# Kernel tuning notes

Measured on AMD Instinct MI355X. Metric: run time of the kernel, lower is better.

Reference implementation:

```python
import jax, jax.numpy as jnp
import numpy as np

N_NODES = 100000
N_EDGES = 1600000
D = 128


def _sage_conv(x, src, dst, W_l, b_l, W_r, num_nodes):
    # gather source-node features along edges, mean-aggregate at destination
    msg_sum = jax.ops.segment_sum(x[src], dst, num_segments=num_nodes)  # [N, D]
    cnt = jax.ops.segment_sum(jnp.ones((src.shape[0], 1), x.dtype), dst,
                              num_segments=num_nodes)                   # [N, 1]
    agg = msg_sum / jnp.maximum(cnt, 1.0)
    # PyG SAGEConv: lin_l(aggregated) + bias + lin_r(self), root linear has no bias
    return agg @ W_l + b_l + x @ W_r


def setup_inputs() -> dict:
    key = jax.random.key(0)
    ks = jax.random.split(key, 8)
    scale = 1.0 / np.sqrt(D)
    x = jax.random.normal(ks[0], (N_NODES, D), dtype=jnp.float32)
    edge_index = jax.random.randint(ks[1], (2, N_EDGES), 0, N_NODES, dtype=jnp.int64)
    W_l1 = jax.random.normal(ks[2], (D, D), dtype=jnp.float32) * scale
    b_l1 = jnp.zeros((D,), dtype=jnp.float32)
    W_r1 = jax.random.normal(ks[3], (D, D), dtype=jnp.float32) * scale
    W_l2 = jax.random.normal(ks[4], (D, D), dtype=jnp.float32) * scale
    b_l2 = jnp.zeros((D,), dtype=jnp.float32)
    W_r2 = jax.random.normal(ks[5], (D, D), dtype=jnp.float32) * scale
    return {"x": x, "edge_index": edge_index, "W_l1": W_l1, "b_l1": b_l1,
            "W_r1": W_r1, "W_l2": W_l2, "b_l2": b_l2, "W_r2": W_r2}


def reference(x, edge_index, W_l1, b_l1, W_r1, W_l2, b_l2, W_r2):
    src, dst = edge_index[0], edge_index[1]
    n = x.shape[0]
    h = jax.nn.relu(_sage_conv(x, src, dst, W_l1, b_l1, W_r1, n))
    out = _sage_conv(h, src, dst, W_l2, b_l2, W_r2, n)
    return out
```

## Files before the change

### kernel.cpp

```cpp
#include <hip/hip_runtime.h>
#include <hip/hip_bf16.h>

#define DF 128
#define BSH 7
#define BNODES (1 << BSH)
#define SRCBITS 17
#define SRCMASK ((1u << SRCBITS) - 1u)
#define NBLK 512
#define SLABSH 13
#define NKEYS (BNODES * 16)
#define EBCAP 2560
#define CURSTR 16

typedef __attribute__((ext_vector_type(8))) short short8;
typedef __attribute__((ext_vector_type(4))) float floatx4;

__device__ __forceinline__ unsigned short f2bf(float f) {
  unsigned u = __float_as_uint(f);
  u += 0x7fffu + ((u >> 16) & 1u);
  return (unsigned short)(u >> 16);
}
__device__ __forceinline__ float bflo(unsigned u) { return __uint_as_float(u << 16); }
__device__ __forceinline__ float bfhi(unsigned u) { return __uint_as_float(u & 0xffff0000u); }


__global__ __launch_bounds__(256) void fused_prep(const int* __restrict__ src,
                                                  const int* __restrict__ dst,
                                                  int* __restrict__ cur,
                                                  unsigned* __restrict__ ebuf,
                                                  int e, int nb, int chunk,
                                                  const float* __restrict__ x,
                                                  unsigned short* __restrict__ xb, int n4,
                                                  const float* __restrict__ W0,
                                                  const float* __restrict__ W1,
                                                  const float* __restrict__ W2,
                                                  const float* __restrict__ W3,
                                                  unsigned short* __restrict__ wf) {
  int bid = blockIdx.x, t = threadIdx.x;
  if (bid < NBLK) {
    __shared__ int cnt[1024];
    __shared__ int runb[1024];
    for (int b = t; b < nb; b += 256) cnt[b] = 0;
    __syncthreads();
    int s = bid * chunk, en = min(e, s + chunk);
    int sv[13], dv[13];
    int cntl = 0;
#pragma unroll
    for (int j = 0; j < 13; ++j) {
      int i = s + t + j * 256;
      if (i < en) { sv[j] = src[i]; dv[j] = dst[i]; cntl = j + 1; }
    }
#pragma unroll
    for (int j = 0; j < 13; ++j)
      if (j < cntl) atomicAdd(&cnt[dv[j] >> BSH], 1);
    __syncthreads();
    for (int b = t; b < nb; b += 256) {
      int c = cnt[b];
      runb[b] = (c > 0) ? (b * EBCAP + atomicAdd(&cur[b * CURSTR], c)) : 0;
    }
    __syncthreads();
#pragma unroll
    for (int j = 0; j < 13; ++j)
      if (j < cntl) {
        int d = dv[j];
        int p = atomicAdd(&runb[d >> BSH], 1);
        ebuf[p] = ((unsigned)(d & (BNODES - 1)) << SRCBITS) | (unsigned)sv[j];
      }
  } else if (bid < NBLK + 256) {
    int bb = bid - NBLK;
    int m = bb >> 6;
    const float* W = (m == 0) ? W0 : (m == 1) ? W1 : (m == 2) ? W2 : W3;
    int tt = (bb & 63) * 256 + t;
    int j = tt & 7, lane = (tt >> 3) & 63, ktnt = tt >> 9;
    int nt = ktnt & 7, kt = ktnt >> 3;
    int k = kt * 32 + (lane >> 4) * 8 + j;
    int ncol = nt * 16 + (lane & 15);
    wf[m * 16384 + tt] = f2bf(W[k * DF + ncol]);
  } else {
    int i = (bid - NBLK - 256) * 256 + t;
    if (i < n4) {
      float4 v = ((const float4*)x)[i];
      union { unsigned short u[4]; uint2 d; } o;
      o.u[0] = f2bf(v.x); o.u[1] = f2bf(v.y); o.u[2] = f2bf(v.z); o.u[3] = f2bf(v.w);
      ((uint2*)xb)[i] = o.d;
    }
  }
}

__global__ __launch_bounds__(256) void fill_fine(const unsigned* __restrict__ ebuf,
                                                 const int* __restrict__ cend,
                                                 int* __restrict__ rs,
                                                 int* __restrict__ csr, int n) {
  __shared__ int hist[NKEYS];
  __shared__ int cur[NKEYS];
  __shared__ int wsum[4];
  int b = blockIdx.x;
  int t = threadIdx.x;
  for (int i = t; i < NKEYS; i += 256) hist[i] = 0;
  __syncthreads();
  int s = b * EBCAP, e = s + cend[b * CURSTR];
  for (int i = s + t; i < e; i += 256) {
    unsigned p = ebuf[i];
    int key = (int)((p >> SRCBITS) << 4) | (int)((p & SRCMASK) >> SLABSH);
    atomicAdd(&hist[key], 1);
  }
  __syncthreads();
  int v[8], sum = 0;
#pragma unroll
  for (int j = 0; j < 8; ++j) { v[j] = hist[t * 8 + j]; sum += v[j]; }
  int lane = t & 63, wid = t >> 6;
  int S = sum;
#pragma unroll
  for (int o = 1; o < 64; o <<= 1) {
    int u = __shfl_up(S, o);
    if (lane >= o) S += u;
  }
  if (lane == 63) wsum[wid] = S;
  __syncthreads();
  if (wid == 0 && lane < 4) {
    int ws = wsum[lane];
#pragma unroll
    for (int o = 1; o < 4; o <<= 1) {
      int u = __shfl_up(ws, o);
      if (lane >= o) ws += u;
    }
    wsum[lane] = ws;
  }
  __syncthreads();
  int base = (S - sum) + ((wid > 0) ? wsum[wid - 1] : 0);
#pragma unroll
  for (int j = 0; j < 8; ++j) { cur[t * 8 + j] = base; base += v[j]; }
  __syncthreads();
  if (t < BNODES) {
    int g = (b << BSH) + t;
    if (g < n) {
      int endoff = (t == BNODES - 1) ? (e - s) : cur[(t + 1) << 4];
      rs[g] = s + endoff;
    }
  }
  __syncthreads();
  for (int i = s + t; i < e; i += 256) {
    unsigned p = ebuf[i];
    int key = (int)((p >> SRCBITS) << 4) | (int)((p & SRCMASK) >> SLABSH);
    int r = atomicAdd(&cur[key], 1);
    csr[s + r] = (int)(p & SRCMASK);
  }
}

__global__ __launch_bounds__(256) void agg_pull(const uint4* __restrict__ feat,
                                                const int* __restrict__ rs,
                                                const int* __restrict__ csr,
                                                uint4* __restrict__ out, int n) {
  int node = (blockIdx.x * 256 + threadIdx.x) >> 6;
  if (node >= n) return;
  int lane = threadIdx.x & 63;
  int g = lane >> 4, l = lane & 15;
  int s = (node & (BNODES - 1)) ? rs[node - 1] : (node >> BSH) * EBCAP;
  int e = rs[node];
  float a0 = 0.f, a1 = 0.f, a2 = 0.f, a3 = 0.f;
  float a4 = 0.f, a5 = 0.f, a6 = 0.f, a7 = 0.f;
  int em1 = e - 1;
  for (int i = s; i < e; i += 16) {
    int i0 = i + g, i1 = i + g + 4, i2 = i + g + 8, i3 = i + g + 12;
    int c0 = csr[min(i0, em1)];
    int c1 = csr[min(i1, em1)];
    int c2 = csr[min(i2, em1)];
    int c3 = csr[min(i3, em1)];
    uint4 u0 = feat[c0 * 16 + l];
    uint4 u1 = feat[c1 * 16 + l];
    uint4 u2 = feat[c2 * 16 + l];
    uint4 u3 = feat[c3 * 16 + l];
    if (i0 >= e) { u0.x = 0u; u0.y = 0u; u0.z = 0u; u0.w = 0u; }
    if (i1 >= e) { u1.x = 0u; u1.y = 0u; u1.z = 0u; u1.w = 0u; }
    if (i2 >= e) { u2.x = 0u; u2.y = 0u; u2.z = 0u; u2.w = 0u; }
    if (i3 >= e) { u3.x = 0u; u3.y = 0u; u3.z = 0u; u3.w = 0u; }
    a0 += bflo(u0.x); a1 += bfhi(u0.x); a2 += bflo(u0.y); a3 += bfhi(u0.y);
    a4 += bflo(u0.z); a5 += bfhi(u0.z); a6 += bflo(u0.w); a7 += bfhi(u0.w);
    a0 += bflo(u1.x); a1 += bfhi(u1.x); a2 += bflo(u1.y); a3 += bfhi(u1.y);
    a4 += bflo(u1.z); a5 += bfhi(u1.z); a6 += bflo(u1.w); a7 += bfhi(u1.w);
    a0 += bflo(u2.x); a1 += bfhi(u2.x); a2 += bflo(u2.y); a3 += bfhi(u2.y);
    a4 += bflo(u2.z); a5 += bfhi(u2.z); a6 += bflo(u2.w); a7 += bfhi(u2.w);
    a0 += bflo(u3.x); a1 += bfhi(u3.x); a2 += bflo(u3.y); a3 += bfhi(u3.y);
    a4 += bflo(u3.z); a5 += bfhi(u3.z); a6 += bflo(u3.w); a7 += bfhi(u3.w);
  }
  a0 += __shfl_xor(a0, 16); a0 += __shfl_xor(a0, 32);
  a1 += __shfl_xor(a1, 16); a1 += __shfl_xor(a1, 32);
  a2 += __shfl_xor(a2, 16); a2 += __shfl_xor(a2, 32);
  a3 += __shfl_xor(a3, 16); a3 += __shfl_xor(a3, 32);
  a4 += __shfl_xor(a4, 16); a4 += __shfl_xor(a4, 32);
  a5 += __shfl_xor(a5, 16); a5 += __shfl_xor(a5, 32);
  a6 += __shfl_xor(a6, 16); a6 += __shfl_xor(a6, 32);
  a7 += __shfl_xor(a7, 16); a7 += __shfl_xor(a7, 32);
  if (g == 0) {
    float sc = 1.0f / (float)max(e - s, 1);
    uint4 o;
    o.x = (unsigned)f2bf(a0 * sc) | ((unsigned)f2bf(a1 * sc) << 16);
    o.y = (unsigned)f2bf(a2 * sc) | ((unsigned)f2bf(a3 * sc) << 16);
    o.z = (unsigned)f2bf(a4 * sc) | ((unsigned)f2bf(a5 * sc) << 16);
    o.w = (unsigned)f2bf(a6 * sc) | ((unsigned)f2bf(a7 * sc) << 16);
    out[node * 16 + l] = o;
  }
}

__global__ __launch_bounds__(256) void gemm_sage(const unsigned short* __restrict__ Aagg,
                                                 const unsigned short* __restrict__ Aself,
                                                 const unsigned short* __restrict__ WFl,
                                                 const unsigned short* __restrict__ WFr,
                                                 const float* __restrict__ bias,
                                                 void* __restrict__ outp, int n,
                                                 int relu_out_bf16) {
  __shared__ unsigned short Wsl[DF * DF];
  __shared__ unsigned short Wsr[DF * DF];
  int t = threadIdx.x;
  {
    const uint4* wl4 = (const uint4*)WFl;
    const uint4* wr4 = (const uint4*)WFr;
    uint4* sl4 = (uint4*)Wsl;
    uint4* sr4 = (uint4*)Wsr;
#pragma unroll
    for (int i = 0; i < 8; ++i) {
      sl4[i * 256 + t] = wl4[i * 256 + t];
      sr4[i * 256 + t] = wr4[i * 256 + t];
    }
  }
  __syncthreads();

  int wave = t >> 6;
  int lane = t & 63;
  int l16 = lane & 15, quad = lane >> 4;
  int rbase = (blockIdx.x * 4 + wave) * 32;
  if (rbase >= n) return;

  floatx4 acc[2][8];
#pragma unroll
  for (int a = 0; a < 2; ++a)
#pragma unroll
    for (int b = 0; b < 8; ++b) acc[a][b] = (floatx4)0.0f;

  int r0 = min(rbase + l16, n - 1);
  int r1 = min(rbase + 16 + l16, n - 1);

#pragma unroll
  for (int s = 0; s < 2; ++s) {
    const unsigned short* A = s ? Aself : Aagg;
    const unsigned short* W = s ? Wsr : Wsl;
    short8 a0[4], a1[4];
#pragma unroll
    for (int kt = 0; kt < 4; ++kt) {
      a0[kt] = *(const short8*)(A + r0 * DF + kt * 32 + quad * 8);
      a1[kt] = *(const short8*)(A + r1 * DF + kt * 32 + quad * 8);
    }
#pragma unroll
    for (int kt = 0; kt < 4; ++kt) {
#pragma unroll
      for (int nt = 0; nt < 8; ++nt) {
        short8 bf = *(const short8*)(W + (((kt * 8 + nt) * 64) + lane) * 8);
        acc[0][nt] = __builtin_amdgcn_mfma_f32_16x16x32_bf16(a0[kt], bf, acc[0][nt], 0, 0, 0);
        acc[1][nt] = __builtin_amdgcn_mfma_f32_16x16x32_bf16(a1[kt], bf, acc[1][nt], 0, 0, 0);
      }
    }
  }

  float bv[8];
#pragma unroll
  for (int nt = 0; nt < 8; ++nt) bv[nt] = bias[nt * 16 + l16];

  if (relu_out_bf16) {
    unsigned short* O = (unsigned short*)outp;
#pragma unroll
    for (int rb = 0; rb < 2; ++rb)
#pragma unroll
      for (int i = 0; i < 4; ++i) {
        int row = rbase + rb * 16 + quad * 4 + i;
        if (row < n) {
#pragma unroll
          for (int nt = 0; nt < 8; ++nt) {
            float v = acc[rb][nt][i] + bv[nt];
            O[row * DF + nt * 16 + l16] = f2bf(fmaxf(v, 0.0f));
          }
        }
      }
  } else {
    float* O = (float*)outp;
#pragma unroll
    for (int rb = 0; rb < 2; ++rb)
#pragma unroll
      for (int i = 0; i < 4; ++i) {
        int row = rbase + rb * 16 + quad * 4 + i;
        if (row < n) {
#pragma unroll
          for (int nt = 0; nt < 8; ++nt)
            O[row * DF + nt * 16 + l16] = acc[rb][nt][i] + bv[nt];
        }
      }
  }
}


extern "C" void kernel_launch(void* const* d_in, const int* in_sizes, int n_in,
                              void* d_out, int out_size, void* d_ws, size_t ws_size,
                              hipStream_t stream) {
  const float* x   = (const float*)d_in[0];
  const int*   ei  = (const int*)d_in[1];
  const float* Wl1 = (const float*)d_in[2];
  const float* bl1 = (const float*)d_in[3];
  const float* Wr1 = (const float*)d_in[4];
  const float* Wl2 = (const float*)d_in[5];
  const float* bl2 = (const float*)d_in[6];
  const float* Wr2 = (const float*)d_in[7];

  int n = in_sizes[0] / DF;
  int e = in_sizes[1] / 2;
  const int* srcv = ei;
  const int* dstv = ei + e;
  int nb = (n + BNODES - 1) >> BSH;
  int chunk = (e + NBLK - 1) / NBLK;

  char* ws = (char*)d_ws;
  size_t off = 0;
  auto alloc = [&](size_t bytes) {
    void* p = ws + off;
    off = (off + bytes + 255) & ~(size_t)255;
    return p;
  };
  int* cur   = (int*)alloc((size_t)nb * CURSTR * 4);
  int* rs    = (int*)alloc((size_t)n * 4);
  unsigned* ebuf = (unsigned*)alloc((size_t)nb * EBCAP * 4);
  int* csr   = (int*)alloc((size_t)nb * EBCAP * 4);
  unsigned short* xb   = (unsigned short*)alloc((size_t)n * DF * 2);
  unsigned short* hb   = (unsigned short*)alloc((size_t)n * DF * 2);
  unsigned short* aggb = (unsigned short*)alloc((size_t)n * DF * 2);
  unsigned short* wf   = (unsigned short*)alloc(4 * DF * DF * 2);
  unsigned short* wfl1 = wf;
  unsigned short* wfr1 = wf + 16384;
  unsigned short* wfl2 = wf + 32768;
  unsigned short* wfr2 = wf + 49152;

  int n4 = n * DF / 4;
  int cb = (n4 + 255) / 256;
  hipMemsetAsync(cur, 0, (size_t)nb * CURSTR * 4, stream);
  fused_prep<<<NBLK + 256 + cb, 256, 0, stream>>>(srcv, dstv, cur, ebuf, e, nb, chunk,
                                                  x, xb, n4, Wl1, Wr1, Wl2, Wr2, wf);
  fill_fine<<<nb, 256, 0, stream>>>(ebuf, cur, rs, csr, n);

  agg_pull<<<(n * 64 + 255) / 256, 256, 0, stream>>>((const uint4*)xb, rs, csr,
                                                     (uint4*)aggb, n);
  gemm_sage<<<(n + 127) / 128, 256, 0, stream>>>(aggb, xb, wfl1, wfr1, bl1, hb, n, 1);
  agg_pull<<<(n * 64 + 255) / 256, 256, 0, stream>>>((const uint4*)hb, rs, csr,
                                                     (uint4*)aggb, n);
  gemm_sage<<<(n + 127) / 128, 256, 0, stream>>>(aggb, hb, wfl2, wfr2, bl2, d_out, n, 0);
}
```

Measured before the change: 308.8 us.

## Pad CSR segments to multiples of eight with a zero sentinel row

Each node's CSR segment is padded to a multiple of eight entries, and the padding points at an extra zeroed feature row (index n). This lets the aggregation loop drop its bounds clamps and masking and load neighbour indices as int2. The bucketing and histogram kernels now read edges with vectorized int4 loads, and the partition block count and bucket capacity are changed. The cost is extra wasted gathers on padding entries, one or two extra memsets, and a larger EBCAP that bounds the number of edges per bucket.

```diff
diff --git a/kernel.cpp b/kernel.cpp
--- a/kernel.cpp
+++ b/kernel.cpp
@@ -6,10 +6,10 @@
 #define BNODES (1 << BSH)
 #define SRCBITS 17
 #define SRCMASK ((1u << SRCBITS) - 1u)
-#define NBLK 512
+#define NBLK 256
 #define SLABSH 13
 #define NKEYS (BNODES * 16)
-#define EBCAP 2560
+#define EBCAP 2944
 #define CURSTR 16
 
 typedef __attribute__((ext_vector_type(8))) short short8;
@@ -43,29 +43,50 @@
     for (int b = t; b < nb; b += 256) cnt[b] = 0;
     __syncthreads();
     int s = bid * chunk, en = min(e, s + chunk);
-    int sv[13], dv[13];
-    int cntl = 0;
-#pragma unroll
-    for (int j = 0; j < 13; ++j) {
-      int i = s + t + j * 256;
-      if (i < en) { sv[j] = src[i]; dv[j] = dst[i]; cntl = j + 1; }
-    }
-#pragma unroll
-    for (int j = 0; j < 13; ++j)
-      if (j < cntl) atomicAdd(&cnt[dv[j] >> BSH], 1);
+    int nv = en - s;
+    if (nv <= 0) return;
+    int nv4 = (nv + 3) >> 2;
+    const int4* d4p = (const int4*)(dst + s);
+    const int4* s4p = (const int4*)(src + s);
+    for (int i4 = t; i4 < nv4; i4 += 256) {
+      int4 d4 = d4p[i4];
+      int base = i4 << 2;
+      if (base + 0 < nv) atomicAdd(&cnt[d4.x >> BSH], 1);
+      if (base + 1 < nv) atomicAdd(&cnt[d4.y >> BSH], 1);
+      if (base + 2 < nv) atomicAdd(&cnt[d4.z >> BSH], 1);
+      if (base + 3 < nv) atomicAdd(&cnt[d4.w >> BSH], 1);
+    }
     __syncthreads();
     for (int b = t; b < nb; b += 256) {
       int c = cnt[b];
       runb[b] = (c > 0) ? (b * EBCAP + atomicAdd(&cur[b * CURSTR], c)) : 0;
     }
     __syncthreads();
-#pragma unroll
-    for (int j = 0; j < 13; ++j)
-      if (j < cntl) {
-        int d = dv[j];
+    for (int i4 = t; i4 < nv4; i4 += 256) {
+      int4 d4 = d4p[i4];
+      int4 sv4 = s4p[i4];
+      int base = i4 << 2;
+      if (base + 0 < nv) {
+        int d = d4.x;
         int p = atomicAdd(&runb[d >> BSH], 1);
-        ebuf[p] = ((unsigned)(d & (BNODES - 1)) << SRCBITS) | (unsigned)sv[j];
-      }
+        ebuf[p] = ((unsigned)(d & (BNODES - 1)) << SRCBITS) | (unsigned)sv4.x;
+      }
+      if (base + 1 < nv) {
+        int d = d4.y;
+        int p = atomicAdd(&runb[d >> BSH], 1);
+        ebuf[p] = ((unsigned)(d & (BNODES - 1)) << SRCBITS) | (unsigned)sv4.y;
+      }
+      if (base + 2 < nv) {
+        int d = d4.z;
+        int p = atomicAdd(&runb[d >> BSH], 1);
+        ebuf[p] = ((unsigned)(d & (BNODES - 1)) << SRCBITS) | (unsigned)sv4.z;
+      }
+      if (base + 3 < nv) {
+        int d = d4.w;
+        int p = atomicAdd(&runb[d >> BSH], 1);
+        ebuf[p] = ((unsigned)(d & (BNODES - 1)) << SRCBITS) | (unsigned)sv4.w;
+      }
+    }
   } else if (bid < NBLK + 256) {
     int bb = bid - NBLK;
     int m = bb >> 6;
@@ -98,18 +119,27 @@
   int t = threadIdx.x;
   for (int i = t; i < NKEYS; i += 256) hist[i] = 0;
   __syncthreads();
-  int s = b * EBCAP, e = s + cend[b * CURSTR];
-  for (int i = s + t; i < e; i += 256) {
-    unsigned p = ebuf[i];
-    int key = (int)((p >> SRCBITS) << 4) | (int)((p & SRCMASK) >> SLABSH);
-    atomicAdd(&hist[key], 1);
-  }
-  __syncthreads();
-  int v[8], sum = 0;
-#pragma unroll
-  for (int j = 0; j < 8; ++j) { v[j] = hist[t * 8 + j]; sum += v[j]; }
+  int s = b * EBCAP;
+  int len = cend[b * CURSTR];
+  int len4 = (len + 3) >> 2;
+  const uint4* e4p = (const uint4*)(ebuf + s);
+  for (int i4 = t; i4 < len4; i4 += 256) {
+    uint4 p4 = e4p[i4];
+    int base = i4 << 2;
+    if (base + 0 < len) atomicAdd(&hist[(int)((p4.x >> SRCBITS) << 4) | (int)((p4.x & SRCMASK) >> SLABSH)], 1);
+    if (base + 1 < len) atomicAdd(&hist[(int)((p4.y >> SRCBITS) << 4) | (int)((p4.y & SRCMASK) >> SLABSH)], 1);
+    if (base + 2 < len) atomicAdd(&hist[(int)((p4.z >> SRCBITS) << 4) | (int)((p4.z & SRCMASK) >> SLABSH)], 1);
+    if (base + 3 < len) atomicAdd(&hist[(int)((p4.w >> SRCBITS) << 4) | (int)((p4.w & SRCMASK) >> SLABSH)], 1);
+  }
+  __syncthreads();
+  int d = 0;
+  if (t < BNODES) {
+#pragma unroll
+    for (int j = 0; j < 16; ++j) d += hist[t * 16 + j];
+  }
+  int p = (d + 7) & ~7;
   int lane = t & 63, wid = t >> 6;
-  int S = sum;
+  int S = p;
 #pragma unroll
   for (int o = 1; o < 64; o <<= 1) {
     int u = __shfl_up(S, o);
@@ -127,23 +157,40 @@
     wsum[lane] = ws;
   }
   __syncthreads();
-  int base = (S - sum) + ((wid > 0) ? wsum[wid - 1] : 0);
-#pragma unroll
-  for (int j = 0; j < 8; ++j) { cur[t * 8 + j] = base; base += v[j]; }
-  __syncthreads();
+  int nodebase = (S - p) + ((wid > 0) ? wsum[wid - 1] : 0);
   if (t < BNODES) {
+    int off = nodebase;
+#pragma unroll
+    for (int j = 0; j < 16; ++j) { cur[t * 16 + j] = off; off += hist[t * 16 + j]; }
     int g = (b << BSH) + t;
-    if (g < n) {
-      int endoff = (t == BNODES - 1) ? (e - s) : cur[(t + 1) << 4];
-      rs[g] = s + endoff;
-    }
-  }
-  __syncthreads();
-  for (int i = s + t; i < e; i += 256) {
-    unsigned p = ebuf[i];
-    int key = (int)((p >> SRCBITS) << 4) | (int)((p & SRCMASK) >> SLABSH);
-    int r = atomicAdd(&cur[key], 1);
-    csr[s + r] = (int)(p & SRCMASK);
+    if (g < n) rs[g] = s + nodebase + d;
+    int pe = nodebase + p;
+    for (int k = nodebase + d; k < pe; ++k) csr[s + k] = n;
+  }
+  __syncthreads();
+  for (int i4 = t; i4 < len4; i4 += 256) {
+    uint4 p4 = e4p[i4];
+    int base = i4 << 2;
+    if (base + 0 < len) {
+      int key = (int)((p4.x >> SRCBITS) << 4) | (int)((p4.x & SRCMASK) >> SLABSH);
+      int r = atomicAdd(&cur[key], 1);
+      csr[s + r] = (int)(p4.x & SRCMASK);
+    }
+    if (base + 1 < len) {
+      int key = (int)((p4.y >> SRCBITS) << 4) | (int)((p4.y & SRCMASK) >> SLABSH);
+      int r = atomicAdd(&cur[key], 1);
+      csr[s + r] = (int)(p4.y & SRCMASK);
+    }
+    if (base + 2 < len) {
+      int key = (int)((p4.z >> SRCBITS) << 4) | (int)((p4.z & SRCMASK) >> SLABSH);
+      int r = atomicAdd(&cur[key], 1);
+      csr[s + r] = (int)(p4.z & SRCMASK);
+    }
+    if (base + 3 < len) {
+      int key = (int)((p4.w >> SRCBITS) << 4) | (int)((p4.w & SRCMASK) >> SLABSH);
+      int r = atomicAdd(&cur[key], 1);
+      csr[s + r] = (int)(p4.w & SRCMASK);
+    }
   }
 }
 
@@ -155,33 +202,19 @@
   if (node >= n) return;
   int lane = threadIdx.x & 63;
   int g = lane >> 4, l = lane & 15;
-  int s = (node & (BNODES - 1)) ? rs[node - 1] : (node >> BSH) * EBCAP;
   int e = rs[node];
+  int s = (node & (BNODES - 1)) ? ((rs[node - 1] + 7) & ~7)
+                                : (node >> BSH) * EBCAP;
   float a0 = 0.f, a1 = 0.f, a2 = 0.f, a3 = 0.f;
   float a4 = 0.f, a5 = 0.f, a6 = 0.f, a7 = 0.f;
-  int em1 = e - 1;
-  for (int i = s; i < e; i += 16) {
-    int i0 = i + g, i1 = i + g + 4, i2 = i + g + 8, i3 = i + g + 12;
-    int c0 = csr[min(i0, em1)];
-    int c1 = csr[min(i1, em1)];
-    int c2 = csr[min(i2, em1)];
-    int c3 = csr[min(i3, em1)];
-    uint4 u0 = feat[c0 * 16 + l];
-    uint4 u1 = feat[c1 * 16 + l];
-    uint4 u2 = feat[c2 * 16 + l];
-    uint4 u3 = feat[c3 * 16 + l];
-    if (i0 >= e) { u0.x = 0u; u0.y = 0u; u0.z = 0u; u0.w = 0u; }
-    if (i1 >= e) { u1.x = 0u; u1.y = 0u; u1.z = 0u; u1.w = 0u; }
-    if (i2 >= e) { u2.x = 0u; u2.y = 0u; u2.z = 0u; u2.w = 0u; }
-    if (i3 >= e) { u3.x = 0u; u3.y = 0u; u3.z = 0u; u3.w = 0u; }
+  for (int i = s; i < e; i += 8) {
+    int2 c = *(const int2*)(csr + i + (g << 1));
+    uint4 u0 = feat[c.x * 16 + l];
+    uint4 u1 = feat[c.y * 16 + l];
     a0 += bflo(u0.x); a1 += bfhi(u0.x); a2 += bflo(u0.y); a3 += bfhi(u0.y);
     a4 += bflo(u0.z); a5 += bfhi(u0.z); a6 += bflo(u0.w); a7 += bfhi(u0.w);
     a0 += bflo(u1.x); a1 += bfhi(u1.x); a2 += bflo(u1.y); a3 += bfhi(u1.y);
     a4 += bflo(u1.z); a5 += bfhi(u1.z); a6 += bflo(u1.w); a7 += bfhi(u1.w);
-    a0 += bflo(u2.x); a1 += bfhi(u2.x); a2 += bflo(u2.y); a3 += bfhi(u2.y);
-    a4 += bflo(u2.z); a5 += bfhi(u2.z); a6 += bflo(u2.w); a7 += bfhi(u2.w);
-    a0 += bflo(u3.x); a1 += bfhi(u3.x); a2 += bflo(u3.y); a3 += bfhi(u3.y);
-    a4 += bflo(u3.z); a5 += bfhi(u3.z); a6 += bflo(u3.w); a7 += bfhi(u3.w);
   }
   a0 += __shfl_xor(a0, 16); a0 += __shfl_xor(a0, 32);
   a1 += __shfl_xor(a1, 16); a1 += __shfl_xor(a1, 32);
@@ -314,7 +347,7 @@
   const int* srcv = ei;
   const int* dstv = ei + e;
   int nb = (n + BNODES - 1) >> BSH;
-  int chunk = (e + NBLK - 1) / NBLK;
+  int chunk = (((e + NBLK - 1) / NBLK) + 3) & ~3;
 
   char* ws = (char*)d_ws;
   size_t off = 0;
@@ -327,8 +360,8 @@
   int* rs    = (int*)alloc((size_t)n * 4);
   unsigned* ebuf = (unsigned*)alloc((size_t)nb * EBCAP * 4);
   int* csr   = (int*)alloc((size_t)nb * EBCAP * 4);
-  unsigned short* xb   = (unsigned short*)alloc((size_t)n * DF * 2);
-  unsigned short* hb   = (unsigned short*)alloc((size_t)n * DF * 2);
+  unsigned short* xb   = (unsigned short*)alloc((size_t)(n + 1) * DF * 2);
+  unsigned short* hb   = (unsigned short*)alloc((size_t)(n + 1) * DF * 2);
   unsigned short* aggb = (unsigned short*)alloc((size_t)n * DF * 2);
   unsigned short* wf   = (unsigned short*)alloc(4 * DF * DF * 2);
   unsigned short* wfl1 = wf;
@@ -339,6 +372,8 @@
   int n4 = n * DF / 4;
   int cb = (n4 + 255) / 256;
   hipMemsetAsync(cur, 0, (size_t)nb * CURSTR * 4, stream);
+  hipMemsetAsync(xb + (size_t)n * DF, 0, DF * 2, stream);
+  hipMemsetAsync(hb + (size_t)n * DF, 0, DF * 2, stream);
   fused_prep<<<NBLK + 256 + cb, 256, 0, stream>>>(srcv, dstv, cur, ebuf, e, nb, chunk,
                                                   x, xb, n4, Wl1, Wr1, Wl2, Wr2, wf);
   fill_fine<<<nb, 256, 0, stream>>>(ebuf, cur, rs, csr, n);
```

Measured after the change: 306.4 us. No clear change (-0.8%).
